# Kernel optimization log

Hardware: AMD Instinct MI355X
Metric: run time of the kernel (lower is better)

## Reference

```python
import jax, jax.numpy as jnp
import numpy as np

N, C, T, V = 128, 64, 128, 25   # batch, channels (in==out), frames, joints
R = 8                            # rel_channels = in_channels // rel_reduction
H = 12                           # SE hidden dim for joint attention (~V//2)


def setup_inputs() -> dict:
    key = jax.random.key(0)
    ks = jax.random.split(key, 8)
    w = lambda shape, k: jax.random.normal(k, shape, jnp.float32) * 0.05
    return {
        "x": jax.random.normal(ks[0], (N, C, T, V), jnp.float32),
        "A": jax.random.normal(ks[1], (V, V), jnp.float32) * 0.1,
        "w1": w((R, C), ks[2]), "b1": jnp.zeros((R,), jnp.float32),
        "w2": w((R, C), ks[3]), "b2": jnp.zeros((R,), jnp.float32),
        "w4": w((C, R), ks[4]), "b4": jnp.zeros((C,), jnp.float32),
        "se_w1": w((H, V), ks[5]), "se_b1": jnp.zeros((H,), jnp.float32),
        "se_w2": w((V, H), ks[6]), "se_b2": jnp.zeros((V,), jnp.float32),
    }


def reference(x, A, w1, b1, w2, b2, w4, b4, se_w1, se_b1, se_w2, se_b2):
    alpha = 1.0
    # conv1/conv2 are 1x1 convs; mean over T commutes with the linear map,
    # so pool first then project (saves a (N,R,T,V) intermediate).
    xm = x.mean(axis=2)                                     # (N,C,V)
    x1 = jnp.einsum('rc,ncv->nrv', w1, xm) + b1[None, :, None]
    x2 = jnp.einsum('rc,ncv->nrv', w2, xm) + b2[None, :, None]
    # channel-wise relation: broadcast diff + tanh  -> (N,R,V,V)
    rel = jnp.tanh(x1[:, :, :, None] - x2[:, :, None, :])
    # conv4 (1x1) lifts R->C, scale by alpha, add static adjacency
    Adyn = jnp.einsum('or,nruv->nouv', w4, rel) + b4[None, :, None, None]
    Adyn = Adyn * alpha + A[None, None]                     # (N,C,V,V)
    # DRJointSpa: SE attention over joints (pool C,T -> FC -> ReLU -> FC -> sigmoid)
    s = x.mean(axis=(1, 2))                                 # (N,V)
    h = jax.nn.relu(jnp.einsum('hv,nv->nh', se_w1, s) + se_b1)
    a = jax.nn.sigmoid(jnp.einsum('vh,nh->nv', se_w2, h) + se_b2)
    x3 = x * a[:, None, None, :]                            # (N,C,T,V)
    # per-channel graph aggregation over joints
    return jnp.einsum('ncuv,nctv->nctu', Adyn, x3)
```

## Files before the change

kernel.cpp:

```cpp
#include <hip/hip_runtime.h>
#include <hip/hip_bf16.h>

#define NN 128
#define CC 64
#define TT 128
#define VV 25
#define RR 8
#define HH 12
#define TPAD 132

__global__ __launch_bounds__(256) void kA_tmean(const float* __restrict__ x,
                                                float* __restrict__ xm) {
    const int blk = blockIdx.x;
    const int tid = threadIdx.x;
    __shared__ float st[TT * VV];
    __shared__ float ps[8 * VV];

    const float4* xb4 = (const float4*)(x + (size_t)blk * (TT * VV));
    float4* st4 = (float4*)st;
    for (int i = tid; i < (TT * VV) / 4; i += 256) st4[i] = xb4[i];
    __syncthreads();

    if (tid < 200) {
        const int v = tid % VV, tseg = tid / VV;
        float s = 0.f;
        const int base = tseg * 16 * VV + v;
#pragma unroll
        for (int i = 0; i < 16; i++) s += st[base + i * VV];
        ps[tseg * VV + v] = s;
    }
    __syncthreads();
    if (tid < VV) {
        float s = 0.f;
#pragma unroll
        for (int k = 0; k < 8; k++) s += ps[k * VV + tid];
        xm[(size_t)blk * VV + tid] = s * (1.f / TT);
    }
}

__global__ __launch_bounds__(256) void kB_small(
    const float* __restrict__ xm,
    const float* __restrict__ w1, const float* __restrict__ b1,
    const float* __restrict__ w2, const float* __restrict__ b2,
    const float* __restrict__ sw1, const float* __restrict__ sb1,
    const float* __restrict__ sw2, const float* __restrict__ sb2,
    float* __restrict__ a_out, float* __restrict__ rel_out) {
    const int n = blockIdx.x;
    const int tid = threadIdx.x;
    __shared__ float lxm[CC * VV];
    __shared__ float ls[VV];
    __shared__ float lh[HH];
    __shared__ float l1[RR * VV];
    __shared__ float l2[RR * VV];

    for (int i = tid; i < CC * VV; i += 256) lxm[i] = xm[(size_t)n * CC * VV + i];
    __syncthreads();

    if (tid < VV) {
        float s = 0.f;
        for (int c = 0; c < CC; c++) s += lxm[c * VV + tid];
        ls[tid] = s * (1.f / CC);
    }
    if (tid < RR * VV) {
        int r = tid / VV, v = tid % VV;
        float s1 = b1[r], s2 = b2[r];
        for (int c = 0; c < CC; c++) {
            float xv = lxm[c * VV + v];
            s1 += w1[r * CC + c] * xv;
            s2 += w2[r * CC + c] * xv;
        }
        l1[tid] = s1;
        l2[tid] = s2;
    }
    __syncthreads();

    if (tid < HH) {
        float h = sb1[tid];
        for (int v = 0; v < VV; v++) h += sw1[tid * VV + v] * ls[v];
        lh[tid] = fmaxf(h, 0.f);
    }
    __syncthreads();

    if (tid < VV) {
        float z = sb2[tid];
        for (int j = 0; j < HH; j++) z += sw2[tid * HH + j] * lh[j];
        a_out[(size_t)n * VV + tid] = 1.f / (1.f + expf(-z));
    }

    for (int idx = tid; idx < RR * VV * VV; idx += 256) {
        int r = idx / (VV * VV);
        int rem = idx % (VV * VV);
        int u = rem / VV, v = rem % VV;
        rel_out[(size_t)n * RR * VV * VV + idx] = tanhf(l1[r * VV + u] - l2[r * VV + v]);
    }
}

__global__ __launch_bounds__(256) void kC_main(
    const float* __restrict__ x, const float* __restrict__ A,
    const float* __restrict__ w4, const float* __restrict__ b4,
    const float* __restrict__ rel, const float* __restrict__ av,
    float* __restrict__ out) {
    const int blk = blockIdx.x;
    const int n = blk / CC;
    const int c = blk % CC;
    const int tid = threadIdx.x;

    __shared__ float ad[28 * 28];
    __shared__ float xs[28 * TPAD];
    float* os = xs;

    float w4r[RR];
#pragma unroll
    for (int r = 0; r < RR; r++) w4r[r] = w4[c * RR + r];
    const float b4c = b4[c];

    for (int uv = tid; uv < 28 * 28; uv += 256) {
        int u = uv / 28, v = uv % 28;
        float val = 0.f;
        if (u < VV && v < VV) {
            val = b4c + A[u * VV + v];
            const float* rp = rel + (size_t)n * RR * VV * VV + u * VV + v;
#pragma unroll
            for (int r = 0; r < RR; r++) val += w4r[r] * rp[r * VV * VV];
            val *= av[(size_t)n * VV + v];
        }
        ad[uv] = val;
    }

    const float4* xb4 = (const float4*)(x + (size_t)blk * (TT * VV));
    for (int i = tid; i < (TT * VV) / 4; i += 256) {
        float4 q = xb4[i];
        int lin = i * 4;
        float vals[4] = {q.x, q.y, q.z, q.w};
#pragma unroll
        for (int k = 0; k < 4; k++) {
            int l = lin + k;
            int t = l / VV, v = l - t * VV;
            xs[v * TPAD + t] = vals[k];
        }
    }
    for (int i = tid; i < 3 * TPAD; i += 256) xs[25 * TPAD + i] = 0.f;
    __syncthreads();

    const int ug = tid >> 5;
    const int tg = tid & 31;
    const int u0 = ug * 4;
    const int t0 = tg * 4;
    float acc[4][4];
#pragma unroll
    for (int dt = 0; dt < 4; dt++)
#pragma unroll
        for (int j = 0; j < 4; j++) acc[dt][j] = 0.f;

    if (ug < 7) {
#pragma unroll
        for (int vb = 0; vb < 7; vb++) {
            float4 a4[4];
            float4 x4[4];
#pragma unroll
            for (int j = 0; j < 4; j++) a4[j] = *(const float4*)&ad[(u0 + j) * 28 + vb * 4];
#pragma unroll
            for (int vi = 0; vi < 4; vi++) x4[vi] = *(const float4*)&xs[(vb * 4 + vi) * TPAD + t0];
            const float* xv = (const float*)&x4[0];
#pragma unroll
            for (int dt = 0; dt < 4; dt++) {
#pragma unroll
                for (int j = 0; j < 4; j++) {
                    acc[dt][j] += a4[j].x * xv[0 * 4 + dt];
                    acc[dt][j] += a4[j].y * xv[1 * 4 + dt];
                    acc[dt][j] += a4[j].z * xv[2 * 4 + dt];
                    acc[dt][j] += a4[j].w * xv[3 * 4 + dt];
                }
            }
        }
    }
    __syncthreads();

    if (ug < 7) {
#pragma unroll
        for (int dt = 0; dt < 4; dt++) {
#pragma unroll
            for (int j = 0; j < 4; j++) {
                int u = u0 + j;
                if (u < VV) os[(t0 + dt) * VV + u] = acc[dt][j];
            }
        }
    }
    __syncthreads();

    float4* ob4 = (float4*)(out + (size_t)blk * (TT * VV));
    const float4* os4 = (const float4*)os;
    for (int i = tid; i < (TT * VV) / 4; i += 256) ob4[i] = os4[i];
}

extern "C" void kernel_launch(void* const* d_in, const int* in_sizes, int n_in,
                              void* d_out, int out_size, void* d_ws, size_t ws_size,
                              hipStream_t stream) {
    const float* x   = (const float*)d_in[0];
    const float* A   = (const float*)d_in[1];
    const float* w1  = (const float*)d_in[2];
    const float* b1  = (const float*)d_in[3];
    const float* w2  = (const float*)d_in[4];
    const float* b2  = (const float*)d_in[5];
    const float* w4  = (const float*)d_in[6];
    const float* b4  = (const float*)d_in[7];
    const float* sw1 = (const float*)d_in[8];
    const float* sb1 = (const float*)d_in[9];
    const float* sw2 = (const float*)d_in[10];
    const float* sb2 = (const float*)d_in[11];
    float* out = (float*)d_out;

    float* ws = (float*)d_ws;
    float* xm  = ws;
    float* a_s = xm + (size_t)NN * CC * VV;
    float* rel = a_s + (size_t)NN * VV;

    kA_tmean<<<NN * CC, 256, 0, stream>>>(x, xm);
    kB_small<<<NN, 256, 0, stream>>>(xm, w1, b1, w2, b2, sw1, sb1, sw2, sb2, a_s, rel);
    kC_main<<<NN * CC, 256, 0, stream>>>(x, A, w4, b4, rel, a_s, out);
}
```

Baseline: 247.4 us.

## Pad rel layout, vectorize Adyn build, trim padded joint work in main kernel

The rel tensor is stored with rows padded to 28 so the main kernel can build the dynamic adjacency with float4 loads, one thread per four output columns. The x tile loads are issued up front into registers before the adjacency computation, and the transpose scatter uses incremental index arithmetic instead of per-element divides. The aggregation drops the zero-padded 25th–28th joint rows and columns, handling the last joint as a special case in a separate warp group, which shrinks shared memory. This adds register pressure and branchier code for the tail joint.

```diff
diff --git a/kernel.cpp b/kernel.cpp
--- a/kernel.cpp
+++ b/kernel.cpp
@@ -8,6 +8,9 @@
 #define RR 8
 #define HH 12
 #define TPAD 132
+#define RELP 28
+#define RELR (VV*RELP)
+#define RELN (RR*RELR)
 
 __global__ __launch_bounds__(256) void kA_tmean(const float* __restrict__ x,
                                                 float* __restrict__ xm) {
@@ -87,11 +90,14 @@
         a_out[(size_t)n * VV + tid] = 1.f / (1.f + expf(-z));
     }
 
-    for (int idx = tid; idx < RR * VV * VV; idx += 256) {
-        int r = idx / (VV * VV);
-        int rem = idx % (VV * VV);
-        int u = rem / VV, v = rem % VV;
-        rel_out[(size_t)n * RR * VV * VV + idx] = tanhf(l1[r * VV + u] - l2[r * VV + v]);
+    for (int idx = tid; idx < RELN; idx += 256) {
+        int r = idx / RELR;
+        int rem = idx - r * RELR;
+        int u = rem / RELP;
+        int v = rem - u * RELP;
+        float val = 0.f;
+        if (v < VV) val = tanhf(l1[r * VV + u] - l2[r * VV + v]);
+        rel_out[(size_t)n * RELN + idx] = val;
     }
 }
 
@@ -101,45 +107,76 @@
     const float* __restrict__ rel, const float* __restrict__ av,
     float* __restrict__ out) {
     const int blk = blockIdx.x;
-    const int n = blk / CC;
-    const int c = blk % CC;
+    const int n = blk >> 6;
+    const int c = blk & (CC - 1);
     const int tid = threadIdx.x;
 
-    __shared__ float ad[28 * 28];
-    __shared__ float xs[28 * TPAD];
+    __shared__ __align__(16) float ad[VV * RELP];
+    __shared__ __align__(16) float xs[VV * TPAD];
     float* os = xs;
+
+    const float4* xb4 = (const float4*)(x + (size_t)blk * (TT * VV));
+    float4 q0 = xb4[tid];
+    float4 q1 = xb4[tid + 256];
+    float4 q2 = xb4[tid + 512];
+    float4 q3;
+    if (tid < 32) q3 = xb4[tid + 768];
 
     float w4r[RR];
 #pragma unroll
     for (int r = 0; r < RR; r++) w4r[r] = w4[c * RR + r];
     const float b4c = b4[c];
 
-    for (int uv = tid; uv < 28 * 28; uv += 256) {
-        int u = uv / 28, v = uv % 28;
-        float val = 0.f;
-        if (u < VV && v < VV) {
-            val = b4c + A[u * VV + v];
-            const float* rp = rel + (size_t)n * RR * VV * VV + u * VV + v;
-#pragma unroll
-            for (int r = 0; r < RR; r++) val += w4r[r] * rp[r * VV * VV];
-            val *= av[(size_t)n * VV + v];
-        }
-        ad[uv] = val;
-    }
-
-    const float4* xb4 = (const float4*)(x + (size_t)blk * (TT * VV));
-    for (int i = tid; i < (TT * VV) / 4; i += 256) {
-        float4 q = xb4[i];
-        int lin = i * 4;
-        float vals[4] = {q.x, q.y, q.z, q.w};
-#pragma unroll
-        for (int k = 0; k < 4; k++) {
-            int l = lin + k;
-            int t = l / VV, v = l - t * VV;
-            xs[v * TPAD + t] = vals[k];
-        }
-    }
-    for (int i = tid; i < 3 * TPAD; i += 256) xs[25 * TPAD + i] = 0.f;
+    if (tid < VV * 7) {
+        const int u = tid / 7;
+        const int v0 = (tid - u * 7) * 4;
+        const float* rp = rel + (size_t)n * RELN + u * RELP + v0;
+        float s0 = b4c, s1 = b4c, s2 = b4c, s3 = b4c;
+#pragma unroll
+        for (int r = 0; r < RR; r++) {
+            const float4 rq = *(const float4*)(rp + r * RELR);
+            s0 += w4r[r] * rq.x;
+            s1 += w4r[r] * rq.y;
+            s2 += w4r[r] * rq.z;
+            s3 += w4r[r] * rq.w;
+        }
+        const int c0 = v0;
+        const int c1 = min(v0 + 1, VV - 1);
+        const int c2 = min(v0 + 2, VV - 1);
+        const int c3 = min(v0 + 3, VV - 1);
+        const float* Ar = A + u * VV;
+        const float* avp = av + (size_t)n * VV;
+        float4 o;
+        o.x = (s0 + Ar[c0]) * avp[c0];
+        o.y = (s1 + Ar[c1]) * avp[c1];
+        o.z = (s2 + Ar[c2]) * avp[c2];
+        o.w = (s3 + Ar[c3]) * avp[c3];
+        *(float4*)&ad[u * RELP + v0] = o;
+    }
+
+    {
+        int lin = tid * 4;
+        int t = lin / VV;
+        int v = lin - t * VV;
+#define SCAT4(q)                                              \
+        {                                                     \
+            int tt = t, vv = v;                               \
+            xs[vv * TPAD + tt] = (q).x;                       \
+            vv++; if (vv == VV) { vv = 0; tt++; }             \
+            xs[vv * TPAD + tt] = (q).y;                       \
+            vv++; if (vv == VV) { vv = 0; tt++; }             \
+            xs[vv * TPAD + tt] = (q).z;                       \
+            vv++; if (vv == VV) { vv = 0; tt++; }             \
+            xs[vv * TPAD + tt] = (q).w;                       \
+        }
+#define ADV1024() { v += 24; t += 40; if (v >= VV) { v -= VV; t += 1; } }
+        SCAT4(q0); ADV1024();
+        SCAT4(q1); ADV1024();
+        SCAT4(q2); ADV1024();
+        if (tid < 32) SCAT4(q3);
+#undef SCAT4
+#undef ADV1024
+    }
     __syncthreads();
 
     const int ug = tid >> 5;
@@ -152,13 +189,13 @@
 #pragma unroll
         for (int j = 0; j < 4; j++) acc[dt][j] = 0.f;
 
-    if (ug < 7) {
-#pragma unroll
-        for (int vb = 0; vb < 7; vb++) {
+    if (ug < 6) {
+#pragma unroll
+        for (int vb = 0; vb < 6; vb++) {
             float4 a4[4];
             float4 x4[4];
 #pragma unroll
-            for (int j = 0; j < 4; j++) a4[j] = *(const float4*)&ad[(u0 + j) * 28 + vb * 4];
+            for (int j = 0; j < 4; j++) a4[j] = *(const float4*)&ad[(u0 + j) * RELP + vb * 4];
 #pragma unroll
             for (int vi = 0; vi < 4; vi++) x4[vi] = *(const float4*)&xs[(vb * 4 + vi) * TPAD + t0];
             const float* xv = (const float*)&x4[0];
@@ -173,24 +210,65 @@
                 }
             }
         }
-    }
-    __syncthreads();
-
-    if (ug < 7) {
-#pragma unroll
-        for (int dt = 0; dt < 4; dt++) {
-#pragma unroll
-            for (int j = 0; j < 4; j++) {
-                int u = u0 + j;
-                if (u < VV) os[(t0 + dt) * VV + u] = acc[dt][j];
+        {
+            const float a0 = ad[(u0 + 0) * RELP + 24];
+            const float a1 = ad[(u0 + 1) * RELP + 24];
+            const float a2 = ad[(u0 + 2) * RELP + 24];
+            const float a3 = ad[(u0 + 3) * RELP + 24];
+            float4 xt = *(const float4*)&xs[24 * TPAD + t0];
+            const float* xtp = (const float*)&xt;
+#pragma unroll
+            for (int dt = 0; dt < 4; dt++) {
+                const float xvd = xtp[dt];
+                acc[dt][0] += a0 * xvd;
+                acc[dt][1] += a1 * xvd;
+                acc[dt][2] += a2 * xvd;
+                acc[dt][3] += a3 * xvd;
             }
         }
+    } else if (ug == 6) {
+#pragma unroll
+        for (int vb = 0; vb < 6; vb++) {
+            float4 a40 = *(const float4*)&ad[24 * RELP + vb * 4];
+            float4 x4[4];
+#pragma unroll
+            for (int vi = 0; vi < 4; vi++) x4[vi] = *(const float4*)&xs[(vb * 4 + vi) * TPAD + t0];
+            const float* xv = (const float*)&x4[0];
+#pragma unroll
+            for (int dt = 0; dt < 4; dt++) {
+                acc[dt][0] += a40.x * xv[0 * 4 + dt];
+                acc[dt][0] += a40.y * xv[1 * 4 + dt];
+                acc[dt][0] += a40.z * xv[2 * 4 + dt];
+                acc[dt][0] += a40.w * xv[3 * 4 + dt];
+            }
+        }
+        {
+            const float a0 = ad[24 * RELP + 24];
+            float4 xt = *(const float4*)&xs[24 * TPAD + t0];
+            const float* xtp = (const float*)&xt;
+#pragma unroll
+            for (int dt = 0; dt < 4; dt++) acc[dt][0] += a0 * xtp[dt];
+        }
+    }
+    __syncthreads();
+
+    if (ug < 6) {
+#pragma unroll
+        for (int dt = 0; dt < 4; dt++)
+#pragma unroll
+            for (int j = 0; j < 4; j++) os[(t0 + dt) * VV + u0 + j] = acc[dt][j];
+    } else if (ug == 6) {
+#pragma unroll
+        for (int dt = 0; dt < 4; dt++) os[(t0 + dt) * VV + 24] = acc[dt][0];
     }
     __syncthreads();
 
     float4* ob4 = (float4*)(out + (size_t)blk * (TT * VV));
     const float4* os4 = (const float4*)os;
-    for (int i = tid; i < (TT * VV) / 4; i += 256) ob4[i] = os4[i];
+    ob4[tid]       = os4[tid];
+    ob4[tid + 256] = os4[tid + 256];
+    ob4[tid + 512] = os4[tid + 512];
+    if (tid < 32) ob4[tid + 768] = os4[tid + 768];
 }
 
 extern "C" void kernel_launch(void* const* d_in, const int* in_sizes, int n_in,
```

Measured after the change: 232.3 us. -6.1%, faster.

## Compute joint aggregation with split-bf16 MFMA instead of FP32 FMA loops

Applied to the files above, without the earlier changes.

The main per-(n,c) kernel now splits x and the dynamic adjacency into bf16 high and low parts and computes the 128x25x25 product with three 16x16x32 bf16 MFMA passes (hi*hi, hi*lo, lo*hi), approximating FP32 accuracy. The rel buffer is padded to 28 columns so adjacency assembly can use float4 loads, and the output copy loop is unrolled. The aim is to offload the small GEMM to matrix cores. In exchange it adds conversion work per element and some precision loss from dropping the lo*lo term.

```diff
diff --git a/kernel.cpp b/kernel.cpp
--- a/kernel.cpp
+++ b/kernel.cpp
@@ -7,7 +7,21 @@
 #define VV 25
 #define RR 8
 #define HH 12
-#define TPAD 132
+#define RELP 28
+#define RELR (VV*RELP)
+#define RELN (RR*RELR)
+#define KP 40
+
+typedef __attribute__((ext_vector_type(8))) short short8;
+typedef __attribute__((ext_vector_type(4))) float f32x4;
+
+__device__ __forceinline__ unsigned int f2bf(float f) {
+    unsigned int u = __builtin_bit_cast(unsigned int, f);
+    return (u + 0x7FFFu + ((u >> 16) & 1u)) >> 16;
+}
+__device__ __forceinline__ float bf2f(unsigned int b) {
+    return __builtin_bit_cast(float, b << 16);
+}
 
 __global__ __launch_bounds__(256) void kA_tmean(const float* __restrict__ x,
                                                 float* __restrict__ xm) {
@@ -87,11 +101,14 @@
         a_out[(size_t)n * VV + tid] = 1.f / (1.f + expf(-z));
     }
 
-    for (int idx = tid; idx < RR * VV * VV; idx += 256) {
-        int r = idx / (VV * VV);
-        int rem = idx % (VV * VV);
-        int u = rem / VV, v = rem % VV;
-        rel_out[(size_t)n * RR * VV * VV + idx] = tanhf(l1[r * VV + u] - l2[r * VV + v]);
+    for (int idx = tid; idx < RELN; idx += 256) {
+        int r = idx / RELR;
+        int rem = idx - r * RELR;
+        int u = rem / RELP;
+        int v = rem - u * RELP;
+        float val = 0.f;
+        if (v < VV) val = tanhf(l1[r * VV + u] - l2[r * VV + v]);
+        rel_out[(size_t)n * RELN + idx] = val;
     }
 }
 
@@ -101,88 +118,134 @@
     const float* __restrict__ rel, const float* __restrict__ av,
     float* __restrict__ out) {
     const int blk = blockIdx.x;
-    const int n = blk / CC;
-    const int c = blk % CC;
+    const int n = blk >> 6;
+    const int c = blk & (CC - 1);
     const int tid = threadIdx.x;
 
-    __shared__ float ad[28 * 28];
-    __shared__ float xs[28 * TPAD];
-    float* os = xs;
-
-    float w4r[RR];
-#pragma unroll
-    for (int r = 0; r < RR; r++) w4r[r] = w4[c * RR + r];
-    const float b4c = b4[c];
-
-    for (int uv = tid; uv < 28 * 28; uv += 256) {
-        int u = uv / 28, v = uv % 28;
-        float val = 0.f;
-        if (u < VV && v < VV) {
-            val = b4c + A[u * VV + v];
-            const float* rp = rel + (size_t)n * RR * VV * VV + u * VV + v;
-#pragma unroll
-            for (int r = 0; r < RR; r++) val += w4r[r] * rp[r * VV * VV];
-            val *= av[(size_t)n * VV + v];
-        }
-        ad[uv] = val;
-    }
-
-    const float4* xb4 = (const float4*)(x + (size_t)blk * (TT * VV));
-    for (int i = tid; i < (TT * VV) / 4; i += 256) {
-        float4 q = xb4[i];
-        int lin = i * 4;
-        float vals[4] = {q.x, q.y, q.z, q.w};
-#pragma unroll
-        for (int k = 0; k < 4; k++) {
-            int l = lin + k;
-            int t = l / VV, v = l - t * VV;
-            xs[v * TPAD + t] = vals[k];
-        }
-    }
-    for (int i = tid; i < 3 * TPAD; i += 256) xs[25 * TPAD + i] = 0.f;
-    __syncthreads();
-
-    const int ug = tid >> 5;
-    const int tg = tid & 31;
-    const int u0 = ug * 4;
-    const int t0 = tg * 4;
-    float acc[4][4];
-#pragma unroll
-    for (int dt = 0; dt < 4; dt++)
-#pragma unroll
-        for (int j = 0; j < 4; j++) acc[dt][j] = 0.f;
-
-    if (ug < 7) {
-#pragma unroll
-        for (int vb = 0; vb < 7; vb++) {
-            float4 a4[4];
-            float4 x4[4];
-#pragma unroll
-            for (int j = 0; j < 4; j++) a4[j] = *(const float4*)&ad[(u0 + j) * 28 + vb * 4];
-#pragma unroll
-            for (int vi = 0; vi < 4; vi++) x4[vi] = *(const float4*)&xs[(vb * 4 + vi) * TPAD + t0];
-            const float* xv = (const float*)&x4[0];
-#pragma unroll
-            for (int dt = 0; dt < 4; dt++) {
-#pragma unroll
-                for (int j = 0; j < 4; j++) {
-                    acc[dt][j] += a4[j].x * xv[0 * 4 + dt];
-                    acc[dt][j] += a4[j].y * xv[1 * 4 + dt];
-                    acc[dt][j] += a4[j].z * xv[2 * 4 + dt];
-                    acc[dt][j] += a4[j].w * xv[3 * 4 + dt];
-                }
+    __shared__ __align__(16) unsigned short xsb[2][TT * KP];
+    __shared__ __align__(16) unsigned short adb[2][32 * KP];
+    float* os = (float*)&xsb[0][0];
+
+    const float* xg = x + (size_t)blk * (TT * VV);
+
+    {
+        int t = tid / 13;
+        int p = tid - t * 13;
+#pragma unroll
+        for (int it = 0; it < 7; ++it) {
+            if (it < 6 || t < TT) {
+                const float* row = xg + t * VV + 2 * p;
+                float f0 = row[0];
+                float f1 = row[(p < 12) ? 1 : 0];
+                if (p >= 12) f1 = 0.f;
+                unsigned int h0 = f2bf(f0);
+                unsigned int l0 = f2bf(f0 - bf2f(h0));
+                unsigned int h1 = f2bf(f1);
+                unsigned int l1 = f2bf(f1 - bf2f(h1));
+                *(unsigned int*)&xsb[0][t * KP + 2 * p] = h0 | (h1 << 16);
+                *(unsigned int*)&xsb[1][t * KP + 2 * p] = l0 | (l1 << 16);
             }
-        }
-    }
-    __syncthreads();
-
-    if (ug < 7) {
-#pragma unroll
-        for (int dt = 0; dt < 4; dt++) {
-#pragma unroll
-            for (int j = 0; j < 4; j++) {
-                int u = u0 + j;
-                if (u < VV) os[(t0 + dt) * VV + u] = acc[dt][j];
+            p += 9; t += 19;
+            if (p >= 13) { p -= 13; ++t; }
+        }
+        for (int i = tid; i < TT * 3; i += 256) {
+            int tt = i / 3, q = i - (i / 3) * 3;
+            *(unsigned int*)&xsb[0][tt * KP + 26 + 2 * q] = 0u;
+            *(unsigned int*)&xsb[1][tt * KP + 26 + 2 * q] = 0u;
+        }
+    }
+
+    {
+        float w4r[RR];
+#pragma unroll
+        for (int r = 0; r < RR; r++) w4r[r] = w4[c * RR + r];
+        const float b4c = b4[c];
+
+        if (tid < VV * 7) {
+            const int u = tid / 7;
+            const int v0 = (tid - u * 7) * 4;
+            const float* rp = rel + (size_t)n * RELN + u * RELP + v0;
+            float s0 = b4c, s1 = b4c, s2 = b4c, s3 = b4c;
+#pragma unroll
+            for (int r = 0; r < RR; r++) {
+                const float4 rq = *(const float4*)(rp + r * RELR);
+                s0 += w4r[r] * rq.x;
+                s1 += w4r[r] * rq.y;
+                s2 += w4r[r] * rq.z;
+                s3 += w4r[r] * rq.w;
+            }
+            const int c0 = v0;
+            const int c1 = min(v0 + 1, VV - 1);
+            const int c2 = min(v0 + 2, VV - 1);
+            const int c3 = min(v0 + 3, VV - 1);
+            const float* Ar = A + u * VV;
+            const float* avp = av + (size_t)n * VV;
+            float o0 = (s0 + Ar[c0]) * avp[c0];
+            float o1 = (s1 + Ar[c1]) * avp[c1];
+            float o2 = (s2 + Ar[c2]) * avp[c2];
+            float o3 = (s3 + Ar[c3]) * avp[c3];
+            unsigned int h0 = f2bf(o0), h1 = f2bf(o1), h2 = f2bf(o2), h3 = f2bf(o3);
+            unsigned int l0 = f2bf(o0 - bf2f(h0));
+            unsigned int l1 = f2bf(o1 - bf2f(h1));
+            unsigned int l2 = f2bf(o2 - bf2f(h2));
+            unsigned int l3 = f2bf(o3 - bf2f(h3));
+            *(unsigned int*)&adb[0][u * KP + v0]     = h0 | (h1 << 16);
+            *(unsigned int*)&adb[0][u * KP + v0 + 2] = h2 | (h3 << 16);
+            *(unsigned int*)&adb[1][u * KP + v0]     = l0 | (l1 << 16);
+            *(unsigned int*)&adb[1][u * KP + v0 + 2] = l2 | (l3 << 16);
+        }
+        if (tid < 25 * 6) {
+            int u = tid / 6, q = tid - (tid / 6) * 6;
+            *(unsigned int*)&adb[0][u * KP + 28 + 2 * q] = 0u;
+            *(unsigned int*)&adb[1][u * KP + 28 + 2 * q] = 0u;
+        }
+        for (int i = tid; i < 7 * 20; i += 256) {
+            int rr2 = i / 20, cc2 = i - (i / 20) * 20;
+            *(unsigned int*)&adb[0][(VV + rr2) * KP + 2 * cc2] = 0u;
+            *(unsigned int*)&adb[1][(VV + rr2) * KP + 2 * cc2] = 0u;
+        }
+    }
+    __syncthreads();
+
+    const int wid = tid >> 6;
+    const int lane = tid & 63;
+    const int fr = lane & 15;
+    const int fk = (lane >> 4) * 8;
+
+    f32x4 acc[2][2] = {};
+    short8 ah[2], al[2], bh[2], bl[2];
+#pragma unroll
+    for (int mi = 0; mi < 2; ++mi) {
+        const int m = (wid * 2 + mi) * 16 + fr;
+        ah[mi] = *(const short8*)&xsb[0][m * KP + fk];
+        al[mi] = *(const short8*)&xsb[1][m * KP + fk];
+    }
+#pragma unroll
+    for (int ni = 0; ni < 2; ++ni) {
+        const int nn2 = ni * 16 + fr;
+        bh[ni] = *(const short8*)&adb[0][nn2 * KP + fk];
+        bl[ni] = *(const short8*)&adb[1][nn2 * KP + fk];
+    }
+#pragma unroll
+    for (int mi = 0; mi < 2; ++mi)
+#pragma unroll
+        for (int ni = 0; ni < 2; ++ni) {
+            acc[mi][ni] = __builtin_amdgcn_mfma_f32_16x16x32_bf16(ah[mi], bh[ni], acc[mi][ni], 0, 0, 0);
+            acc[mi][ni] = __builtin_amdgcn_mfma_f32_16x16x32_bf16(ah[mi], bl[ni], acc[mi][ni], 0, 0, 0);
+            acc[mi][ni] = __builtin_amdgcn_mfma_f32_16x16x32_bf16(al[mi], bh[ni], acc[mi][ni], 0, 0, 0);
+        }
+    __syncthreads();
+
+#pragma unroll
+    for (int mi = 0; mi < 2; ++mi) {
+        const int tb = (wid * 2 + mi) * 16 + (lane >> 4) * 4;
+#pragma unroll
+        for (int ni = 0; ni < 2; ++ni) {
+            const int u = ni * 16 + fr;
+            if (u < VV) {
+#pragma unroll
+                for (int r = 0; r < 4; ++r)
+                    os[(tb + r) * VV + u] = acc[mi][ni][r];
             }
         }
     }
@@ -190,7 +253,10 @@
 
     float4* ob4 = (float4*)(out + (size_t)blk * (TT * VV));
     const float4* os4 = (const float4*)os;
-    for (int i = tid; i < (TT * VV) / 4; i += 256) ob4[i] = os4[i];
+    ob4[tid]       = os4[tid];
+    ob4[tid + 256] = os4[tid + 256];
+    ob4[tid + 512] = os4[tid + 512];
+    if (tid < 32) ob4[tid + 768] = os4[tid + 768];
 }
 
 extern "C" void kernel_launch(void* const* d_in, const int* in_sizes, int n_in,
```

After: 229.9 us. -7.1%, faster.
